# Optimization experiments

Measured on AMD Instinct MI355X. Metric: run time of the kernel, lower is better.

## Reference

```python
import jax, jax.numpy as jnp
import numpy as np

ANCHORS = jnp.array([[1.3221, 1.73145], [3.19275, 4.00944], [5.05587, 8.09892],
                     [9.47112, 4.84053], [11.2364, 10.0071]], dtype=jnp.float32)
NUM_ANCHORS = 5
NUM_CLASSES = 20
MAX_BOXES = 50
NOOBJECT_SCALE = 1.0
OBJECT_SCALE = 5.0
COORD_SCALE = 1.0
CLASS_SCALE = 1.0
SIL_THRESH = 0.6


def iou_cwh(b1, b2):
    # boxes as (cx, cy, w, h); matches repo bbox_ious(x1y1x2y2=False)
    x1, y1, w1, h1 = b1[..., 0], b1[..., 1], b1[..., 2], b1[..., 3]
    x2, y2, w2, h2 = b2[..., 0], b2[..., 1], b2[..., 2], b2[..., 3]
    uw = jnp.maximum(x1 + w1 * 0.5, x2 + w2 * 0.5) - jnp.minimum(x1 - w1 * 0.5, x2 - w2 * 0.5)
    uh = jnp.maximum(y1 + h1 * 0.5, y2 + h2 * 0.5) - jnp.minimum(y1 - h1 * 0.5, y2 - h2 * 0.5)
    cw = w1 + w2 - uw
    ch = h1 + h2 - uh
    inter = jnp.where((cw <= 0) | (ch <= 0), 0.0, cw * ch)
    return inter / (w1 * h1 + w2 * h2 - inter)


def setup_inputs() -> dict:
    key = jax.random.key(0)
    k1, k2, k3, k4 = jax.random.split(key, 4)
    nB = 64
    output = jax.random.normal(k1, (nB, NUM_ANCHORS * (5 + NUM_CLASSES), 38, 38), dtype=jnp.float32)
    # target layout per box: (class, x, y, w, h), all normalized; x>0 marks a valid box
    cls_col = jax.random.randint(k2, (nB, MAX_BOXES, 1), 0, NUM_CLASSES).astype(jnp.float32)
    xy = jax.random.uniform(k3, (nB, MAX_BOXES, 2), minval=0.05, maxval=0.95)
    wh = jax.random.uniform(k4, (nB, MAX_BOXES, 2), minval=0.02, maxval=0.3)
    target = jnp.concatenate([cls_col, xy, wh], axis=-1).reshape(nB, MAX_BOXES * 5)
    return {"output": output, "target": target}


def region_loss(output, target):
    nB = output.shape[0]
    nA, nC = NUM_ANCHORS, NUM_CLASSES
    nH, nW = output.shape[2], output.shape[3]
    out = output.reshape(nB, nA, 5 + nC, nH, nW)
    x = jax.nn.sigmoid(out[:, :, 0])
    y = jax.nn.sigmoid(out[:, :, 1])
    w = out[:, :, 2]
    h = out[:, :, 3]
    conf = jax.nn.sigmoid(out[:, :, 4])
    # [nB,nA,nC,nH,nW] -> [nB*nA*nH*nW, nC] (matches torch transpose/view order)
    cls_logits = jnp.transpose(out[:, :, 5:], (0, 1, 3, 4, 2)).reshape(-1, nC)

    sg = jax.lax.stop_gradient
    aw, ah = ANCHORS[:, 0], ANCHORS[:, 1]
    grid_x = jnp.arange(nW, dtype=jnp.float32)[None, None, None, :]
    grid_y = jnp.arange(nH, dtype=jnp.float32)[None, None, :, None]
    px = sg(x) + grid_x
    py = sg(y) + grid_y
    pw = jnp.exp(sg(w)) * aw[None, :, None, None]
    ph = jnp.exp(sg(h)) * ah[None, :, None, None]
    pred_boxes = jnp.stack([px, py, pw, ph], axis=-1)  # [nB,nA,nH,nW,4]

    # ---- build_targets (vectorized) ----
    tgt = sg(target).reshape(nB, MAX_BOXES, 5)
    gcls = tgt[:, :, 0]
    gx = tgt[:, :, 1] * nW
    gy = tgt[:, :, 2] * nH
    gw = tgt[:, :, 3] * nW
    gh = tgt[:, :, 4] * nH
    # loop breaks at first x==0 -> cumulative validity
    valid = jnp.cumprod((tgt[:, :, 1] != 0).astype(jnp.int32), axis=1).astype(bool)

    # silence conf_mask where any-GT IoU > thresh
    pb_flat = pred_boxes.reshape(nB, nA * nH * nW, 4)
    gt_boxes = jnp.stack([gx, gy, gw, gh], axis=-1)  # [nB,50,4]
    ious = iou_cwh(pb_flat[:, :, None, :], gt_boxes[:, None, :, :])  # [nB,nAnc,50]
    ious = jnp.where(valid[:, None, :], ious, 0.0)
    max_iou = jnp.max(ious, axis=2)
    conf_mask = jnp.where(max_iou > SIL_THRESH, 0.0, NOOBJECT_SCALE).reshape(nB, nA, nH, nW)

    # seen < 12800 defaults
    shp = (nB, nA, nH, nW)
    coord_mask = jnp.ones(shp, jnp.float32)
    tx = jnp.full(shp, 0.5, jnp.float32)
    ty = jnp.full(shp, 0.5, jnp.float32)
    tw = jnp.zeros(shp, jnp.float32)
    th = jnp.zeros(shp, jnp.float32)
    tconf = jnp.zeros(shp, jnp.float32)
    tcls = jnp.zeros(shp, jnp.float32)
    cls_mask = jnp.zeros(shp, jnp.float32)

    # best anchor per GT by (0,0,w,h) IoU; argmax keeps first max like the strict '>' loop
    zA = jnp.zeros_like(aw)
    anchor_boxes = jnp.stack([zA, zA, aw, ah], axis=-1)  # [nA,4]
    zg = jnp.zeros_like(gw)
    gt_wh = jnp.stack([zg, zg, gw, gh], axis=-1)  # [nB,50,4]
    a_iou = iou_cwh(gt_wh[:, :, None, :], anchor_boxes[None, None, :, :])  # [nB,50,nA]
    best_n = jnp.argmax(a_iou, axis=2)  # [nB,50]

    gi = jnp.clip(gx.astype(jnp.int32), 0, nW - 1)
    gj = jnp.clip(gy.astype(jnp.int32), 0, nH - 1)
    aw_b = aw[best_n]
    ah_b = ah[best_n]
    tx_v = gx - gi.astype(jnp.float32)
    ty_v = gy - gj.astype(jnp.float32)
    tw_v = jnp.log(gw / aw_b)
    th_v = jnp.log(gh / ah_b)
    b_ix = jnp.arange(nB)
    pred_at = pred_boxes[b_ix[:, None], best_n, gj, gi]  # [nB,50,4]
    iou_gt = iou_cwh(gt_boxes, pred_at)  # [nB,50]

    def step(carry, t):
        cm, clm, tx_, ty_, tw_, th_, tcf, tcl = carry
        bsel = jnp.where(valid[:, t], b_ix, nB)  # out-of-bounds -> dropped
        n, j, i = best_n[:, t], gj[:, t], gi[:, t]
        st = lambda a, v: a.at[bsel, n, j, i].set(v, mode='drop')
        cm = st(cm, jnp.full((nB,), OBJECT_SCALE, jnp.float32))
        clm = st(clm, jnp.ones((nB,), jnp.float32))
        tx_ = st(tx_, tx_v[:, t])
        ty_ = st(ty_, ty_v[:, t])
        tw_ = st(tw_, tw_v[:, t])
        th_ = st(th_, th_v[:, t])
        tcf = st(tcf, iou_gt[:, t])
        tcl = st(tcl, gcls[:, t])
        return (cm, clm, tx_, ty_, tw_, th_, tcf, tcl), None

    init = (conf_mask, cls_mask, tx, ty, tw, th, tconf, tcls)
    (conf_mask, cls_mask, tx, ty, tw, th, tconf, tcls), _ = jax.lax.scan(
        step, init, jnp.arange(MAX_BOXES))

    # ---- losses ----
    cmf = jnp.sqrt(conf_mask)
    loss_x = COORD_SCALE * jnp.sum((x * coord_mask - tx * coord_mask) ** 2) / 2.0
    loss_y = COORD_SCALE * jnp.sum((y * coord_mask - ty * coord_mask) ** 2) / 2.0
    loss_w = COORD_SCALE * jnp.sum((w * coord_mask - tw * coord_mask) ** 2) / 2.0
    loss_h = COORD_SCALE * jnp.sum((h * coord_mask - th * coord_mask) ** 2) / 2.0
    loss_conf = jnp.sum((conf * cmf - tconf * cmf) ** 2) / 2.0
    logp = jax.nn.log_softmax(cls_logits, axis=-1)
    labels = tcls.reshape(-1).astype(jnp.int32)
    ce = -jnp.take_along_axis(logp, labels[:, None], axis=1)[:, 0]
    loss_cls = CLASS_SCALE * jnp.sum(ce * cls_mask.reshape(-1))
    return loss_x + loss_y + loss_w + loss_h + loss_conf + loss_cls


def reference(output, target):
    return region_loss(output, target)
```

## Files before the change

kernel.cpp:

```cpp
#include <hip/hip_runtime.h>
#include <math.h>

#define NA 5
#define NC 20
#define NH 38
#define NW 38
#define MAX_BOXES 50
#define SPAT (NH * NW)
#define CELLS_PER_B (NA * SPAT)
#define TPB 128
#define CELLS_PER_T 4
#define CPB (TPB * CELLS_PER_T)
#define OBJECT_SCALE 5.0f
#define NOOBJECT_SCALE 1.0f

__constant__ float c_aw[NA]  = {1.3221f, 3.19275f, 5.05587f, 9.47112f, 11.2364f};
__constant__ float c_ah[NA]  = {1.73145f, 4.00944f, 8.09892f, 4.84053f, 10.0071f};
__constant__ float c_iaw[NA] = {1.f/1.3221f, 1.f/3.19275f, 1.f/5.05587f, 1.f/9.47112f, 1.f/11.2364f};
__constant__ float c_iah[NA] = {1.f/1.73145f, 1.f/4.00944f, 1.f/8.09892f, 1.f/4.84053f, 1.f/10.0071f};

__device__ __forceinline__ float fexp(float v) { return __expf(v); }
__device__ __forceinline__ float flog(float v) { return __logf(v); }
__device__ __forceinline__ float frcp(float v) { return __builtin_amdgcn_rcpf(v); }
__device__ __forceinline__ float fsig(float v) { return frcp(1.f + __expf(-v)); }

__device__ __forceinline__ float iou_fast(float x1, float y1, float w1, float h1,
                                          float x2, float y2, float w2, float h2) {
  float uw = fmaxf(x1 + w1 * 0.5f, x2 + w2 * 0.5f) - fminf(x1 - w1 * 0.5f, x2 - w2 * 0.5f);
  float uh = fmaxf(y1 + h1 * 0.5f, y2 + h2 * 0.5f) - fminf(y1 - h1 * 0.5f, y2 - h2 * 0.5f);
  float cw = w1 + w2 - uw;
  float ch = h1 + h2 - uh;
  float inter = (cw <= 0.f || ch <= 0.f) ? 0.f : cw * ch;
  return inter * frcp(w1 * h1 + w2 * h2 - inter);
}

__device__ __forceinline__ float iou_wh_exact(float w1, float h1, float w2, float h2) {
  float uw = fmaxf(w1 * 0.5f, w2 * 0.5f) - fminf(-w1 * 0.5f, -w2 * 0.5f);
  float uh = fmaxf(h1 * 0.5f, h2 * 0.5f) - fminf(-h1 * 0.5f, -h2 * 0.5f);
  float cw = w1 + w2 - uw;
  float ch = h1 + h2 - uh;
  float inter = (cw <= 0.f || ch <= 0.f) ? 0.f : cw * ch;
  return inter / (w1 * h1 + w2 * h2 - inter);
}

__global__ __launch_bounds__(TPB) void region_loss_kernel(
    const float* __restrict__ out, const float* __restrict__ target,
    float* __restrict__ outv) {
  const int b = blockIdx.y;
  const int s0 = blockIdx.x * CPB;
  const int tid = threadIdx.x;

  __shared__ float4 sb_lo[MAX_BOXES];
  __shared__ float  sb_ag[MAX_BOXES];
  __shared__ int s_wcnt;
  __shared__ int s_wcell[MAX_BOXES];
  __shared__ float s_wdata[MAX_BOXES][6];
  __shared__ float s_red[2];

  int sC[CELLS_PER_T];
  bool ok[CELLS_PER_T];
  const float* basep[CELLS_PER_T];
  float v0[CELLS_PER_T], v1[CELLS_PER_T], v2[CELLS_PER_T], v3[CELLS_PER_T], v4[CELLS_PER_T];
  float fi[CELLS_PER_T], fj[CELLS_PER_T], paw[CELLS_PER_T], pah[CELLS_PER_T];
#pragma unroll
  for (int q = 0; q < CELLS_PER_T; ++q) {
    int s = s0 + q * TPB + tid;
    ok[q] = (s < CELLS_PER_B);
    int sc = ok[q] ? s : 0;
    sC[q] = ok[q] ? s : -1;
    unsigned a = (unsigned)sc / SPAT;
    unsigned r = (unsigned)sc - a * SPAT;
    unsigned j = r / NW, i = r - j * NW;
    fi[q] = (float)i; fj[q] = (float)j;
    paw[q] = c_aw[a]; pah[q] = c_ah[a];
    const float* bp = out + ((size_t)(b * NA + a) * 25) * SPAT + r;
    basep[q] = bp;
    v0[q] = bp[0];
    v1[q] = bp[SPAT];
    v2[q] = bp[2 * SPAT];
    v3[q] = bp[3 * SPAT];
    v4[q] = bp[4 * SPAT];
  }

  if (tid == TPB - 1) s_wcnt = 0;
  __syncthreads();

  if (tid < 64) {
    int t = tid;
    float cls = 0.f, x = 0.f, y = 0.f, w = 0.f, h = 0.f;
    if (t < MAX_BOXES) {
      const float* tg = target + (size_t)(b * MAX_BOXES + t) * 5;
      cls = tg[0]; x = tg[1]; y = tg[2]; w = tg[3]; h = tg[4];
    }
    unsigned long long nz = __ballot(t < MAX_BOXES && x != 0.f);
    unsigned long long low = (t < 63) ? ((1ull << (t + 1)) - 1ull) : ~0ull;
    bool valid = (t < MAX_BOXES) && ((nz & low) == low);

    float gx = x * NW, gy = y * NH, gw = w * NW, gh = h * NH;

    int best = 0; float bestiou = -1.f;
#pragma unroll
    for (int a2 = 0; a2 < NA; ++a2) {
      float aiou = iou_wh_exact(gw, gh, c_aw[a2], c_ah[a2]);
      if (aiou > bestiou) { bestiou = aiou; best = a2; }
    }
    int gi = min(max((int)gx, 0), NW - 1);
    int gj = min(max((int)gy, 0), NH - 1);

    const float* pb = out + ((size_t)(b * NA + best) * 25) * SPAT + gj * NW + gi;
    float px = fsig(pb[0]) + (float)gi;
    float py = fsig(pb[SPAT]) + (float)gj;
    float pw2 = fexp(pb[2 * SPAT]) * c_aw[best];
    float ph2 = fexp(pb[3 * SPAT]) * c_ah[best];
    float iou_gt = iou_fast(gx, gy, gw, gh, px, py, pw2, ph2);

    int cell = best * SPAT + gj * NW + gi;
    unsigned long long vm = __ballot(valid);
    bool winner = valid;
    for (int tp = 0; tp < MAX_BOXES; ++tp) {
      int c2 = __shfl(cell, tp);
      if (tp > t && ((vm >> tp) & 1ull) && c2 == cell) winner = false;
    }

    if (t < MAX_BOXES) {
      if (valid) {
        sb_lo[t] = make_float4(gx - gw * 0.5f, gx + gw * 0.5f,
                               gy - gh * 0.5f, gy + gh * 0.5f);
        sb_ag[t] = 0.375f * (gw * gh);
      } else {
        sb_lo[t] = make_float4(1e30f, 1e30f, 1e30f, 1e30f);
        sb_ag[t] = 0.f;
      }
      if (winner && cell >= s0 && cell < s0 + CPB) {
        int k = atomicAdd(&s_wcnt, 1);
        s_wcell[k] = cell;
        s_wdata[k][0] = gx - (float)gi;
        s_wdata[k][1] = gy - (float)gj;
        s_wdata[k][2] = flog(gw * c_iaw[best]);
        s_wdata[k][3] = flog(gh * c_iah[best]);
        s_wdata[k][4] = iou_gt;
        s_wdata[k][5] = cls;
      }
    }
  }
  __syncthreads();

  float xs[CELLS_PER_T], ys[CELLS_PER_T], cs[CELLS_PER_T];
  float plx[CELLS_PER_T], phx[CELLS_PER_T], ply[CELLS_PER_T], phy[CELLS_PER_T];
  float ap[CELLS_PER_T], msc[CELLS_PER_T];
#pragma unroll
  for (int q = 0; q < CELLS_PER_T; ++q) {
    xs[q] = fsig(v0[q]);
    ys[q] = fsig(v1[q]);
    cs[q] = fsig(v4[q]);
    float pw = fexp(v2[q]) * paw[q], ph = fexp(v3[q]) * pah[q];
    float px = xs[q] + fi[q], py = ys[q] + fj[q];
    plx[q] = px - pw * 0.5f; phx[q] = px + pw * 0.5f;
    ply[q] = py - ph * 0.5f; phy[q] = py + ph * 0.5f;
    ap[q] = 0.375f * (pw * ph);
    msc[q] = -1e30f;
  }

#pragma unroll
  for (int c0 = 0; c0 < MAX_BOXES; c0 += 10) {
    float4 bl[10]; float bag[10];
#pragma unroll
    for (int u = 0; u < 10; ++u) { bl[u] = sb_lo[c0 + u]; bag[u] = sb_ag[c0 + u]; }
#pragma unroll
    for (int u = 0; u < 10; ++u) {
#pragma unroll
      for (int q = 0; q < CELLS_PER_T; ++q) {
        float cw = fminf(phx[q], bl[u].y) - fmaxf(plx[q], bl[u].x);
        float ch = fminf(phy[q], bl[u].w) - fmaxf(ply[q], bl[u].z);
        cw = fmaxf(cw, 0.f);
        msc[q] = fmaxf(msc[q], fmaf(cw, ch, -bag[u]));
      }
    }
  }

  int cnt = s_wcnt;
  float acc = 0.f;
#pragma unroll
  for (int q = 0; q < CELLS_PER_T; ++q) {
    if (!ok[q]) continue;
    float cmask = (msc[q] > ap[q]) ? 0.f : NOOBJECT_SCALE;
    float tx = 0.5f, ty = 0.5f, tw = 0.f, th = 0.f, tconf = 0.f, clsloss = 0.f;
    for (int k = 0; k < cnt; ++k) {
      if (s_wcell[k] == sC[q]) {
        cmask = OBJECT_SCALE;
        tx = s_wdata[k][0]; ty = s_wdata[k][1];
        tw = s_wdata[k][2]; th = s_wdata[k][3];
        tconf = s_wdata[k][4];
        int label = (int)s_wdata[k][5];
        const float* cb = basep[q] + 5 * SPAT;
        float m = -1e30f, lv = 0.f;
        for (int c = 0; c < NC; ++c) {
          float vv = cb[c * SPAT];
          if (c == label) lv = vv;
          m = fmaxf(m, vv);
        }
        float ssum = 0.f;
        for (int c = 0; c < NC; ++c) ssum += fexp(cb[c * SPAT] - m);
        clsloss = (m + flog(ssum)) - lv;
      }
    }
    float dx = xs[q] - tx, dy = ys[q] - ty, dw = v2[q] - tw, dh = v3[q] - th;
    float dc = cs[q] - tconf;
    acc += 0.5f * (dx * dx + dy * dy + dw * dw + dh * dh + cmask * (dc * dc)) + clsloss;
  }

  for (int o = 32; o > 0; o >>= 1) acc += __shfl_down(acc, o, 64);
  int wid = tid >> 6, lane = tid & 63;
  if (lane == 0) s_red[wid] = acc;
  __syncthreads();
  if (tid == 0)
    atomicAdd(outv, s_red[0] + s_red[1]);
}

extern "C" void kernel_launch(void* const* d_in, const int* in_sizes, int n_in,
                              void* d_out, int out_size, void* d_ws, size_t ws_size,
                              hipStream_t stream) {
  const float* out = (const float*)d_in[0];
  const float* target = (const float*)d_in[1];
  int nB = in_sizes[0] / (NA * (5 + NC) * SPAT);
  int gx = (CELLS_PER_B + CPB - 1) / CPB;
  hipLaunchKernelGGL(region_loss_kernel, dim3(gx, nB), dim3(TPB), 0, stream,
                     out, target, (float*)d_out);
}
```

Before: 107.0 us.

## Replace global atomic accumulation with per-block partials and a reduce kernel

```diff
diff --git a/kernel.cpp b/kernel.cpp
--- a/kernel.cpp
+++ b/kernel.cpp
@@ -8,9 +8,10 @@
 #define MAX_BOXES 50
 #define SPAT (NH * NW)
 #define CELLS_PER_B (NA * SPAT)
-#define TPB 128
-#define CELLS_PER_T 4
+#define TPB 256
+#define CELLS_PER_T 2
 #define CPB (TPB * CELLS_PER_T)
+#define GX ((CELLS_PER_B + CPB - 1) / CPB)
 #define OBJECT_SCALE 5.0f
 #define NOOBJECT_SCALE 1.0f
 
@@ -45,7 +46,7 @@
 
 __global__ __launch_bounds__(TPB) void region_loss_kernel(
     const float* __restrict__ out, const float* __restrict__ target,
-    float* __restrict__ outv) {
+    float* __restrict__ partials) {
   const int b = blockIdx.y;
   const int s0 = blockIdx.x * CPB;
   const int tid = threadIdx.x;
@@ -55,7 +56,7 @@
   __shared__ int s_wcnt;
   __shared__ int s_wcell[MAX_BOXES];
   __shared__ float s_wdata[MAX_BOXES][6];
-  __shared__ float s_red[2];
+  __shared__ float s_red[TPB / 64];
 
   int sC[CELLS_PER_T];
   bool ok[CELLS_PER_T];
@@ -213,8 +214,24 @@
   int wid = tid >> 6, lane = tid & 63;
   if (lane == 0) s_red[wid] = acc;
   __syncthreads();
-  if (tid == 0)
-    atomicAdd(outv, s_red[0] + s_red[1]);
+  if (tid == 0) {
+    float v = 0.f;
+#pragma unroll
+    for (int wdx = 0; wdx < TPB / 64; ++wdx) v += s_red[wdx];
+    partials[blockIdx.y * GX + blockIdx.x] = v;
+  }
+}
+
+__global__ __launch_bounds__(256) void reduce_kernel(
+    const float* __restrict__ partials, int n, float* __restrict__ outv) {
+  float acc = 0.f;
+  for (int i = threadIdx.x; i < n; i += 256) acc += partials[i];
+  for (int o = 32; o > 0; o >>= 1) acc += __shfl_down(acc, o, 64);
+  __shared__ float s_red[4];
+  int wid = threadIdx.x >> 6, lane = threadIdx.x & 63;
+  if (lane == 0) s_red[wid] = acc;
+  __syncthreads();
+  if (threadIdx.x == 0) outv[0] = s_red[0] + s_red[1] + s_red[2] + s_red[3];
 }
 
 extern "C" void kernel_launch(void* const* d_in, const int* in_sizes, int n_in,
@@ -223,7 +240,9 @@
   const float* out = (const float*)d_in[0];
   const float* target = (const float*)d_in[1];
   int nB = in_sizes[0] / (NA * (5 + NC) * SPAT);
-  int gx = (CELLS_PER_B + CPB - 1) / CPB;
-  hipLaunchKernelGGL(region_loss_kernel, dim3(gx, nB), dim3(TPB), 0, stream,
-                     out, target, (float*)d_out);
-}
+  float* partials = (float*)d_ws;
+  hipLaunchKernelGGL(region_loss_kernel, dim3(GX, nB), dim3(TPB), 0, stream,
+                     out, target, partials);
+  hipLaunchKernelGGL(reduce_kernel, dim3(1), dim3(256), 0, stream,
+                     partials, GX * nB, (float*)d_out);
+}
```

Result: slower. 118.4 us (+10.6%).
